# Performance work log

Hardware: AMD Instinct MI355X
Metric: run time of the kernel (lower is better)

The kernel has to match this reference:

```python
import jax, jax.numpy as jnp
import numpy as np

B, C, H, W = 8, 192, 128, 128
FILTERS = (1, 3, 3, 3, 3, 1)
BOUND = 1e-9


def setup_inputs() -> dict:
    key = jax.random.key(0)
    ks = jax.random.split(key, 16)
    d = {"x": jax.random.normal(ks[0], (B, C, H, W), jnp.float32)}
    for i in range(5):
        d[f"m{i}"] = jax.random.normal(ks[1 + i], (C, FILTERS[i + 1], FILTERS[i]), jnp.float32) * 0.5
        d[f"b{i}"] = jax.random.uniform(ks[6 + i], (C, FILTERS[i + 1], 1), jnp.float32, -0.5, 0.5)
    for i in range(4):
        d[f"f{i}"] = jax.random.normal(ks[11 + i], (C, FILTERS[i + 1], 1), jnp.float32) * 0.1
    return d


def _logits_cumulative(x, ms, bs, fs):
    # x: (C, 1, N); per-channel tiny MLP: matmul(softplus(M), x) + b, tanh gate
    logits = x
    for i in range(5):
        logits = jnp.matmul(jax.nn.softplus(ms[i]), logits) + bs[i]
        if i < 4:
            logits = logits + jnp.tanh(fs[i]) * jnp.tanh(logits)
    return logits


def reference(x, m0, m1, m2, m3, m4, b0, b1, b2, b3, b4, f0, f1, f2, f3):
    ms = (m0, m1, m2, m3, m4)
    bs = (b0, b1, b2, b3, b4)
    fs = (f0, f1, f2, f3)
    # quantize: per-sample min/max over (C,H,W), round to 16-bit grid
    x_min = jnp.min(x, axis=(1, 2, 3), keepdims=True)
    x_max = jnp.max(x, axis=(1, 2, 3), keepdims=True)
    xq = jnp.round((x - x_min) * 65535.0 / (x_max - x_min + 1e-12))
    xd = xq / 65535.0  # dequantize
    # permute (B,C,H,W)->(C,B,H,W), reshape to (C,1,N)
    xp = jnp.transpose(xd, (1, 0, 2, 3)).reshape(C, 1, -1)
    lower = _logits_cumulative(xp - 0.5, ms, bs, fs)
    upper = _logits_cumulative(xp + 0.5, ms, bs, fs)
    likelihood = jax.nn.sigmoid(upper) - jax.nn.sigmoid(lower)
    likelihood = jnp.maximum(likelihood, BOUND)  # LowerBound forward
    x_out = jnp.transpose(xp.reshape(C, B, H, W), (1, 0, 2, 3))
    likelihood = jnp.transpose(likelihood.reshape(C, B, H, W), (1, 0, 2, 3))
    return (x_out, likelihood)
```

## Files before the change

kernel.cpp:

```cpp
#include <hip/hip_runtime.h>
#include <math.h>

#define CCH 192
#define BATCH 8
#define HWSZ 16384
#define NPER (CCH * HWSZ)
#define NTOT ((size_t)BATCH * NPER)
#define INV65535 (1.0f / 65535.0f)

#define TABN    8193
#define TABSTR  8196
#define TSCALE  (8192.0f / 65535.0f)

#define WS_WTAB_OFF_FLOATS 64
#define WS_TAB_OFF_BYTES   65536
#define WS_NEEDED (WS_TAB_OFF_BYTES + (size_t)CCH * TABSTR * 4)

__device__ __forceinline__ unsigned f2u_ord(float f) {
    unsigned u = __float_as_uint(f);
    return (u & 0x80000000u) ? ~u : (u | 0x80000000u);
}
__device__ __forceinline__ float u2f_ord(unsigned u) {
    return __uint_as_float((u & 0x80000000u) ? (u ^ 0x80000000u) : ~u);
}
__device__ __forceinline__ float fexp2(float x) { return __builtin_amdgcn_exp2f(x); }
__device__ __forceinline__ float frcp(float x)  { return __builtin_amdgcn_rcpf(x); }
__device__ __forceinline__ float ftanh(float x) {
    return 1.0f - 2.0f * frcp(fexp2(2.8853900817779268f * x) + 1.0f);
}
__device__ __forceinline__ float fsig(float x) {
    return frcp(1.0f + fexp2(-1.4426950408889634f * x));
}

__global__ void setup_kernel(const float* __restrict__ m0, const float* __restrict__ b0,
                             const float* __restrict__ m1, const float* __restrict__ b1,
                             const float* __restrict__ m2, const float* __restrict__ b2,
                             const float* __restrict__ m3, const float* __restrict__ b3,
                             const float* __restrict__ m4, const float* __restrict__ b4,
                             const float* __restrict__ f0, const float* __restrict__ f1,
                             const float* __restrict__ f2, const float* __restrict__ f3,
                             unsigned* __restrict__ mm, float* __restrict__ wtab)
{
    int t = threadIdx.x;
    if (t < 8)             mm[t] = 0xFFFFFFFFu;
    if (t >= 8 && t < 16)  mm[t] = 0u;
    if (t < CCH) {
        float* w = wtab + t * 64;
        #pragma unroll
        for (int i = 0; i < 3; ++i) { float v = m0[t*3+i]; w[i]    = fmaxf(v,0.f)+log1pf(expf(-fabsf(v))); }
        #pragma unroll
        for (int i = 0; i < 9; ++i) { float v = m1[t*9+i]; w[3+i]  = fmaxf(v,0.f)+log1pf(expf(-fabsf(v))); }
        #pragma unroll
        for (int i = 0; i < 9; ++i) { float v = m2[t*9+i]; w[12+i] = fmaxf(v,0.f)+log1pf(expf(-fabsf(v))); }
        #pragma unroll
        for (int i = 0; i < 9; ++i) { float v = m3[t*9+i]; w[21+i] = fmaxf(v,0.f)+log1pf(expf(-fabsf(v))); }
        #pragma unroll
        for (int i = 0; i < 3; ++i) { float v = m4[t*3+i]; w[30+i] = fmaxf(v,0.f)+log1pf(expf(-fabsf(v))); }
        #pragma unroll
        for (int i = 0; i < 3; ++i) w[33+i] = b0[t*3+i];
        #pragma unroll
        for (int i = 0; i < 3; ++i) w[36+i] = b1[t*3+i];
        #pragma unroll
        for (int i = 0; i < 3; ++i) w[39+i] = b2[t*3+i];
        #pragma unroll
        for (int i = 0; i < 3; ++i) w[42+i] = b3[t*3+i];
        w[45] = b4[t];
        #pragma unroll
        for (int i = 0; i < 3; ++i) w[46+i] = tanhf(f0[t*3+i]);
        #pragma unroll
        for (int i = 0; i < 3; ++i) w[49+i] = tanhf(f1[t*3+i]);
        #pragma unroll
        for (int i = 0; i < 3; ++i) w[52+i] = tanhf(f2[t*3+i]);
        #pragma unroll
        for (int i = 0; i < 3; ++i) w[55+i] = tanhf(f3[t*3+i]);
    }
}

#define RED_BLOCKS_PER_SAMPLE 192
__global__ __launch_bounds__(256) void minmax_kernel(const float* __restrict__ x,
                                                     unsigned* __restrict__ mm)
{
    int b   = blockIdx.x / RED_BLOCKS_PER_SAMPLE;
    int blk = blockIdx.x % RED_BLOCKS_PER_SAMPLE;
    const float4* xs = (const float4*)(x + (size_t)b * NPER);
    int base = blk * 4096;
    float mn = INFINITY, mx = -INFINITY;
    #pragma unroll
    for (int i = 0; i < 16; ++i) {
        float4 v = xs[base + i * 256 + threadIdx.x];
        mn = fminf(mn, fminf(fminf(v.x, v.y), fminf(v.z, v.w)));
        mx = fmaxf(mx, fmaxf(fmaxf(v.x, v.y), fmaxf(v.z, v.w)));
    }
    #pragma unroll
    for (int off = 32; off > 0; off >>= 1) {
        mn = fminf(mn, __shfl_down(mn, off, 64));
        mx = fmaxf(mx, __shfl_down(mx, off, 64));
    }
    __shared__ float smn[4], smx[4];
    int wave = threadIdx.x >> 6;
    if ((threadIdx.x & 63) == 0) { smn[wave] = mn; smx[wave] = mx; }
    __syncthreads();
    if (threadIdx.x == 0) {
        #pragma unroll
        for (int i = 1; i < 4; ++i) { mn = fminf(mn, smn[i]); mx = fmaxf(mx, smx[i]); }
        atomicMin(&mm[b],     f2u_ord(mn));
        atomicMax(&mm[8 + b], f2u_ord(mx));
    }
}

__device__ __forceinline__ float eval_mlp(float x, const float* W)
{
    float a0 = fmaf(W[0], x, W[33]);
    float a1 = fmaf(W[1], x, W[34]);
    float a2 = fmaf(W[2], x, W[35]);
    a0 = fmaf(W[46], ftanh(a0), a0);
    a1 = fmaf(W[47], ftanh(a1), a1);
    a2 = fmaf(W[48], ftanh(a2), a2);

    float c0 = fmaf(W[3], a0, fmaf(W[4],  a1, fmaf(W[5],  a2, W[36])));
    float c1 = fmaf(W[6], a0, fmaf(W[7],  a1, fmaf(W[8],  a2, W[37])));
    float c2 = fmaf(W[9], a0, fmaf(W[10], a1, fmaf(W[11], a2, W[38])));
    c0 = fmaf(W[49], ftanh(c0), c0);
    c1 = fmaf(W[50], ftanh(c1), c1);
    c2 = fmaf(W[51], ftanh(c2), c2);

    float d0 = fmaf(W[12], c0, fmaf(W[13], c1, fmaf(W[14], c2, W[39])));
    float d1 = fmaf(W[15], c0, fmaf(W[16], c1, fmaf(W[17], c2, W[40])));
    float d2 = fmaf(W[18], c0, fmaf(W[19], c1, fmaf(W[20], c2, W[41])));
    d0 = fmaf(W[52], ftanh(d0), d0);
    d1 = fmaf(W[53], ftanh(d1), d1);
    d2 = fmaf(W[54], ftanh(d2), d2);

    float e0 = fmaf(W[21], d0, fmaf(W[22], d1, fmaf(W[23], d2, W[42])));
    float e1 = fmaf(W[24], d0, fmaf(W[25], d1, fmaf(W[26], d2, W[43])));
    float e2 = fmaf(W[27], d0, fmaf(W[28], d1, fmaf(W[29], d2, W[44])));
    e0 = fmaf(W[55], ftanh(e0), e0);
    e1 = fmaf(W[56], ftanh(e1), e1);
    e2 = fmaf(W[57], ftanh(e2), e2);

    return fmaf(W[30], e0, fmaf(W[31], e1, fmaf(W[32], e2, W[45])));
}

__device__ __forceinline__ float eval_lik(float d, const float* W)
{
    float lo = eval_mlp(d - 0.5f, W);
    float up = eval_mlp(d + 0.5f, W);
    return fmaxf(fsig(up) - fsig(lo), 1e-9f);
}

__global__ __launch_bounds__(256) void table_kernel(const float* __restrict__ wtab,
                                                    float* __restrict__ tab)
{
    int c = blockIdx.x / 33;
    int j = (blockIdx.x % 33) * 256 + threadIdx.x;
    if (j >= TABN) return;

    float W[58];
    const float* w = wtab + c * 64;
    #pragma unroll
    for (int i = 0; i < 58; ++i) W[i] = w[i];

    float d = (float)j * (1.0f / 8192.0f);
    tab[(size_t)c * TABSTR + j] = eval_lik(d, W);
}

__global__ __launch_bounds__(256) void gather_kernel(const float* __restrict__ x,
                                                     const unsigned* __restrict__ mm,
                                                     const float* __restrict__ tab,
                                                     float* __restrict__ out)
{
    __shared__ __align__(16) float ltab[TABN + 3];

    int c = blockIdx.x >> 3;
    int b = blockIdx.x & 7;
    int t = threadIdx.x;

    const float4* tsrc = (const float4*)(tab + (size_t)c * TABSTR);
    float4* tdst = (float4*)ltab;
    #pragma unroll
    for (int i = 0; i < 8; ++i) tdst[i * 256 + t] = tsrc[i * 256 + t];
    if (t == 0) ltab[8192] = tab[(size_t)c * TABSTR + 8192];
    __syncthreads();

    float mn = u2f_ord(mm[b]);
    float mx = u2f_ord(mm[8 + b]);
    float scale = 65535.0f / (mx - mn + 1e-12f);

    size_t base = ((size_t)b * CCH + c) * HWSZ;
    const float4* xin = (const float4*)(x + base);
    float4* o0 = (float4*)(out + base);
    float4* o1 = (float4*)(out + NTOT + base);

    auto proc = [&](float xi, float& od, float& ol) {
        float kf   = rintf((xi - mn) * scale);
        od         = kf * INV65535;
        float tpos = kf * TSCALE;
        int   j    = (int)tpos;
        j = j > 8191 ? 8191 : j;
        float frac = tpos - (float)j;
        float t0 = ltab[j];
        float t1 = ltab[j + 1];
        ol = fmaxf(fmaf(frac, t1 - t0, t0), 1e-9f);
    };

    #pragma unroll
    for (int i = 0; i < 16; ++i) {
        float4 v = xin[i * 256 + t];
        float4 xd, lk;
        proc(v.x, xd.x, lk.x);
        proc(v.y, xd.y, lk.y);
        proc(v.z, xd.z, lk.z);
        proc(v.w, xd.w, lk.w);
        o0[i * 256 + t] = xd;
        o1[i * 256 + t] = lk;
    }
}

__global__ __launch_bounds__(256) void ebott_main(const float* __restrict__ x,
                                                  const unsigned* __restrict__ mm,
                                                  const float* __restrict__ wtab,
                                                  float* __restrict__ out)
{
    int blk = blockIdx.x;
    int q   = blk & 3;
    int c   = (blk >> 2) % CCH;
    int b   = blk / (4 * CCH);

    float W[58];
    const float* w = wtab + c * 64;
    #pragma unroll
    for (int i = 0; i < 58; ++i) W[i] = w[i];

    float mn = u2f_ord(mm[b]);
    float mx = u2f_ord(mm[8 + b]);
    float scale = 65535.0f / (mx - mn + 1e-12f);

    size_t base = (size_t)(b * CCH + c) * HWSZ + q * 4096;
    const float4* xin = (const float4*)(x + base);
    float4* o0 = (float4*)(out + base);
    float4* o1 = (float4*)(out + NTOT + base);
    int t = threadIdx.x;

    auto proc = [&](float xi, float& od, float& ol) {
        float d = rintf((xi - mn) * scale) * INV65535;
        od = d;
        ol = eval_lik(d, W);
    };

    #pragma unroll
    for (int i = 0; i < 4; ++i) {
        float4 v = xin[i * 256 + t];
        float4 xd, lk;
        proc(v.x, xd.x, lk.x);
        proc(v.y, xd.y, lk.y);
        proc(v.z, xd.z, lk.z);
        proc(v.w, xd.w, lk.w);
        o0[i * 256 + t] = xd;
        o1[i * 256 + t] = lk;
    }
}

extern "C" void kernel_launch(void* const* d_in, const int* in_sizes, int n_in,
                              void* d_out, int out_size, void* d_ws, size_t ws_size,
                              hipStream_t stream)
{
    const float* x  = (const float*)d_in[0];
    const float* m0 = (const float*)d_in[1];
    const float* b0 = (const float*)d_in[2];
    const float* m1 = (const float*)d_in[3];
    const float* b1 = (const float*)d_in[4];
    const float* m2 = (const float*)d_in[5];
    const float* b2 = (const float*)d_in[6];
    const float* m3 = (const float*)d_in[7];
    const float* b3 = (const float*)d_in[8];
    const float* m4 = (const float*)d_in[9];
    const float* b4 = (const float*)d_in[10];
    const float* f0 = (const float*)d_in[11];
    const float* f1 = (const float*)d_in[12];
    const float* f2 = (const float*)d_in[13];
    const float* f3 = (const float*)d_in[14];

    unsigned* mm = (unsigned*)d_ws;
    float* wtab  = (float*)d_ws + WS_WTAB_OFF_FLOATS;
    float* tab   = (float*)((char*)d_ws + WS_TAB_OFF_BYTES);
    float* out   = (float*)d_out;

    setup_kernel<<<1, 256, 0, stream>>>(m0, b0, m1, b1, m2, b2, m3, b3, m4, b4,
                                        f0, f1, f2, f3, mm, wtab);
    minmax_kernel<<<BATCH * RED_BLOCKS_PER_SAMPLE, 256, 0, stream>>>(x, mm);

    if (ws_size >= WS_NEEDED) {
        table_kernel<<<CCH * 33, 256, 0, stream>>>(wtab, tab);
        gather_kernel<<<CCH * BATCH, 256, 0, stream>>>(x, mm, tab, out);
    } else {
        ebott_main<<<BATCH * CCH * 4, 256, 0, stream>>>(x, mm, wtab, out);
    }
}
```

Before: 358.4 us.

## Fuse setup, min/max reduction and table build into one prep kernel

Merges the single-block weight setup, the min/max reduction and the per-channel likelihood table build into one launch. Table blocks now compute their softplus/tanh weights in shared memory, while reduction blocks run alongside them. Min/max initialisation becomes a memset to 0xFF, with the max stored inverted so both reductions use atomicMin. The gather kernel switches to nontemporal loads and stores. This removes two kernel launches and their serialization, at the cost of every table block recomputing its channel weights.

```diff
diff --git a/kernel.cpp b/kernel.cpp
--- a/kernel.cpp
+++ b/kernel.cpp
@@ -16,6 +16,12 @@
 #define WS_TAB_OFF_BYTES   65536
 #define WS_NEEDED (WS_TAB_OFF_BYTES + (size_t)CCH * TABSTR * 4)
 
+#define RED_BLOCKS_PER_SAMPLE 192
+#define MINMAX_BLOCKS (BATCH * RED_BLOCKS_PER_SAMPLE)
+#define TAB_BLOCKS (CCH * 33)
+
+typedef float f4 __attribute__((ext_vector_type(4)));
+
 __device__ __forceinline__ unsigned f2u_ord(float f) {
     unsigned u = __float_as_uint(f);
     return (u & 0x80000000u) ? ~u : (u | 0x80000000u);
@@ -30,82 +36,6 @@
 }
 __device__ __forceinline__ float fsig(float x) {
     return frcp(1.0f + fexp2(-1.4426950408889634f * x));
-}
-
-__global__ void setup_kernel(const float* __restrict__ m0, const float* __restrict__ b0,
-                             const float* __restrict__ m1, const float* __restrict__ b1,
-                             const float* __restrict__ m2, const float* __restrict__ b2,
-                             const float* __restrict__ m3, const float* __restrict__ b3,
-                             const float* __restrict__ m4, const float* __restrict__ b4,
-                             const float* __restrict__ f0, const float* __restrict__ f1,
-                             const float* __restrict__ f2, const float* __restrict__ f3,
-                             unsigned* __restrict__ mm, float* __restrict__ wtab)
-{
-    int t = threadIdx.x;
-    if (t < 8)             mm[t] = 0xFFFFFFFFu;
-    if (t >= 8 && t < 16)  mm[t] = 0u;
-    if (t < CCH) {
-        float* w = wtab + t * 64;
-        #pragma unroll
-        for (int i = 0; i < 3; ++i) { float v = m0[t*3+i]; w[i]    = fmaxf(v,0.f)+log1pf(expf(-fabsf(v))); }
-        #pragma unroll
-        for (int i = 0; i < 9; ++i) { float v = m1[t*9+i]; w[3+i]  = fmaxf(v,0.f)+log1pf(expf(-fabsf(v))); }
-        #pragma unroll
-        for (int i = 0; i < 9; ++i) { float v = m2[t*9+i]; w[12+i] = fmaxf(v,0.f)+log1pf(expf(-fabsf(v))); }
-        #pragma unroll
-        for (int i = 0; i < 9; ++i) { float v = m3[t*9+i]; w[21+i] = fmaxf(v,0.f)+log1pf(expf(-fabsf(v))); }
-        #pragma unroll
-        for (int i = 0; i < 3; ++i) { float v = m4[t*3+i]; w[30+i] = fmaxf(v,0.f)+log1pf(expf(-fabsf(v))); }
-        #pragma unroll
-        for (int i = 0; i < 3; ++i) w[33+i] = b0[t*3+i];
-        #pragma unroll
-        for (int i = 0; i < 3; ++i) w[36+i] = b1[t*3+i];
-        #pragma unroll
-        for (int i = 0; i < 3; ++i) w[39+i] = b2[t*3+i];
-        #pragma unroll
-        for (int i = 0; i < 3; ++i) w[42+i] = b3[t*3+i];
-        w[45] = b4[t];
-        #pragma unroll
-        for (int i = 0; i < 3; ++i) w[46+i] = tanhf(f0[t*3+i]);
-        #pragma unroll
-        for (int i = 0; i < 3; ++i) w[49+i] = tanhf(f1[t*3+i]);
-        #pragma unroll
-        for (int i = 0; i < 3; ++i) w[52+i] = tanhf(f2[t*3+i]);
-        #pragma unroll
-        for (int i = 0; i < 3; ++i) w[55+i] = tanhf(f3[t*3+i]);
-    }
-}
-
-#define RED_BLOCKS_PER_SAMPLE 192
-__global__ __launch_bounds__(256) void minmax_kernel(const float* __restrict__ x,
-                                                     unsigned* __restrict__ mm)
-{
-    int b   = blockIdx.x / RED_BLOCKS_PER_SAMPLE;
-    int blk = blockIdx.x % RED_BLOCKS_PER_SAMPLE;
-    const float4* xs = (const float4*)(x + (size_t)b * NPER);
-    int base = blk * 4096;
-    float mn = INFINITY, mx = -INFINITY;
-    #pragma unroll
-    for (int i = 0; i < 16; ++i) {
-        float4 v = xs[base + i * 256 + threadIdx.x];
-        mn = fminf(mn, fminf(fminf(v.x, v.y), fminf(v.z, v.w)));
-        mx = fmaxf(mx, fmaxf(fmaxf(v.x, v.y), fmaxf(v.z, v.w)));
-    }
-    #pragma unroll
-    for (int off = 32; off > 0; off >>= 1) {
-        mn = fminf(mn, __shfl_down(mn, off, 64));
-        mx = fmaxf(mx, __shfl_down(mx, off, 64));
-    }
-    __shared__ float smn[4], smx[4];
-    int wave = threadIdx.x >> 6;
-    if ((threadIdx.x & 63) == 0) { smn[wave] = mn; smx[wave] = mx; }
-    __syncthreads();
-    if (threadIdx.x == 0) {
-        #pragma unroll
-        for (int i = 1; i < 4; ++i) { mn = fminf(mn, smn[i]); mx = fmaxf(mx, smx[i]); }
-        atomicMin(&mm[b],     f2u_ord(mn));
-        atomicMax(&mm[8 + b], f2u_ord(mx));
-    }
 }
 
 __device__ __forceinline__ float eval_mlp(float x, const float* W)
@@ -148,20 +78,96 @@
     return fmaxf(fsig(up) - fsig(lo), 1e-9f);
 }
 
-__global__ __launch_bounds__(256) void table_kernel(const float* __restrict__ wtab,
-                                                    float* __restrict__ tab)
-{
-    int c = blockIdx.x / 33;
-    int j = (blockIdx.x % 33) * 256 + threadIdx.x;
-    if (j >= TABN) return;
+__device__ __forceinline__ void minmax_block(const float* __restrict__ x,
+                                             unsigned* __restrict__ mm,
+                                             int bid)
+{
+    int b   = bid / RED_BLOCKS_PER_SAMPLE;
+    int blk = bid % RED_BLOCKS_PER_SAMPLE;
+    const f4* xs = (const f4*)(x + (size_t)b * NPER);
+    int base = blk * 4096;
+    float mn = INFINITY, mx = -INFINITY;
+    #pragma unroll
+    for (int i = 0; i < 16; ++i) {
+        f4 v = xs[base + i * 256 + threadIdx.x];
+        mn = fminf(mn, fminf(fminf(v.x, v.y), fminf(v.z, v.w)));
+        mx = fmaxf(mx, fmaxf(fmaxf(v.x, v.y), fmaxf(v.z, v.w)));
+    }
+    #pragma unroll
+    for (int off = 32; off > 0; off >>= 1) {
+        mn = fminf(mn, __shfl_down(mn, off, 64));
+        mx = fmaxf(mx, __shfl_down(mx, off, 64));
+    }
+    __shared__ float smn[4], smx[4];
+    int wave = threadIdx.x >> 6;
+    if ((threadIdx.x & 63) == 0) { smn[wave] = mn; smx[wave] = mx; }
+    __syncthreads();
+    if (threadIdx.x == 0) {
+        #pragma unroll
+        for (int i = 1; i < 4; ++i) { mn = fminf(mn, smn[i]); mx = fmaxf(mx, smx[i]); }
+        atomicMin(&mm[b],     f2u_ord(mn));
+        atomicMin(&mm[8 + b], ~f2u_ord(mx));
+    }
+}
+
+__global__ __launch_bounds__(256) void prep_kernel(
+    const float* __restrict__ x, unsigned* __restrict__ mm,
+    const float* __restrict__ m0, const float* __restrict__ b0,
+    const float* __restrict__ m1, const float* __restrict__ b1,
+    const float* __restrict__ m2, const float* __restrict__ b2,
+    const float* __restrict__ m3, const float* __restrict__ b3,
+    const float* __restrict__ m4, const float* __restrict__ b4,
+    const float* __restrict__ f0, const float* __restrict__ f1,
+    const float* __restrict__ f2, const float* __restrict__ f3,
+    float* __restrict__ tab)
+{
+    if (blockIdx.x < MINMAX_BLOCKS) {
+        minmax_block(x, mm, blockIdx.x);
+        return;
+    }
+    int tb = blockIdx.x - MINMAX_BLOCKS;
+    int c  = tb / 33;
+    int jc = tb % 33;
+    int t  = threadIdx.x;
+
+    __shared__ float sW[58];
+    if (t < 58) {
+        float v;
+        if (t < 33) {
+            if      (t < 3)  v = m0[c * 3 + t];
+            else if (t < 12) v = m1[c * 9 + t - 3];
+            else if (t < 21) v = m2[c * 9 + t - 12];
+            else if (t < 30) v = m3[c * 9 + t - 21];
+            else             v = m4[c * 3 + t - 30];
+            v = fmaxf(v, 0.f) + log1pf(expf(-fabsf(v)));
+        } else if (t < 46) {
+            int i = t - 33;
+            if      (i < 3)  v = b0[c * 3 + i];
+            else if (i < 6)  v = b1[c * 3 + i - 3];
+            else if (i < 9)  v = b2[c * 3 + i - 6];
+            else if (i < 12) v = b3[c * 3 + i - 9];
+            else             v = b4[c];
+        } else {
+            int i = t - 46;
+            if      (i < 3)  v = f0[c * 3 + i];
+            else if (i < 6)  v = f1[c * 3 + i - 3];
+            else if (i < 9)  v = f2[c * 3 + i - 6];
+            else             v = f3[c * 3 + i - 9];
+            v = tanhf(v);
+        }
+        sW[t] = v;
+    }
+    __syncthreads();
 
     float W[58];
-    const float* w = wtab + c * 64;
-    #pragma unroll
-    for (int i = 0; i < 58; ++i) W[i] = w[i];
-
-    float d = (float)j * (1.0f / 8192.0f);
-    tab[(size_t)c * TABSTR + j] = eval_lik(d, W);
+    #pragma unroll
+    for (int i = 0; i < 58; ++i) W[i] = sW[i];
+
+    int j = jc * 256 + t;
+    if (j < TABN) {
+        float d = (float)j * (1.0f / 8192.0f);
+        tab[(size_t)c * TABSTR + j] = eval_lik(d, W);
+    }
 }
 
 __global__ __launch_bounds__(256) void gather_kernel(const float* __restrict__ x,
@@ -175,21 +181,21 @@
     int b = blockIdx.x & 7;
     int t = threadIdx.x;
 
-    const float4* tsrc = (const float4*)(tab + (size_t)c * TABSTR);
-    float4* tdst = (float4*)ltab;
+    const f4* tsrc = (const f4*)(tab + (size_t)c * TABSTR);
+    f4* tdst = (f4*)ltab;
     #pragma unroll
     for (int i = 0; i < 8; ++i) tdst[i * 256 + t] = tsrc[i * 256 + t];
     if (t == 0) ltab[8192] = tab[(size_t)c * TABSTR + 8192];
     __syncthreads();
 
     float mn = u2f_ord(mm[b]);
-    float mx = u2f_ord(mm[8 + b]);
+    float mx = u2f_ord(~mm[8 + b]);
     float scale = 65535.0f / (mx - mn + 1e-12f);
 
     size_t base = ((size_t)b * CCH + c) * HWSZ;
-    const float4* xin = (const float4*)(x + base);
-    float4* o0 = (float4*)(out + base);
-    float4* o1 = (float4*)(out + NTOT + base);
+    const f4* xin = (const f4*)(x + base);
+    f4* o0 = (f4*)(out + base);
+    f4* o1 = (f4*)(out + NTOT + base);
 
     auto proc = [&](float xi, float& od, float& ol) {
         float kf   = rintf((xi - mn) * scale);
@@ -205,14 +211,57 @@
 
     #pragma unroll
     for (int i = 0; i < 16; ++i) {
-        float4 v = xin[i * 256 + t];
-        float4 xd, lk;
-        proc(v.x, xd.x, lk.x);
-        proc(v.y, xd.y, lk.y);
-        proc(v.z, xd.z, lk.z);
-        proc(v.w, xd.w, lk.w);
-        o0[i * 256 + t] = xd;
-        o1[i * 256 + t] = lk;
+        f4 v = __builtin_nontemporal_load(&xin[i * 256 + t]);
+        float in[4] = {v.x, v.y, v.z, v.w};
+        float xd[4], lk[4];
+        #pragma unroll
+        for (int k = 0; k < 4; ++k) proc(in[k], xd[k], lk[k]);
+        f4 vxd = {xd[0], xd[1], xd[2], xd[3]};
+        f4 vlk = {lk[0], lk[1], lk[2], lk[3]};
+        __builtin_nontemporal_store(vxd, &o0[i * 256 + t]);
+        __builtin_nontemporal_store(vlk, &o1[i * 256 + t]);
+    }
+}
+
+__global__ void setup_kernel(const float* __restrict__ m0, const float* __restrict__ b0,
+                             const float* __restrict__ m1, const float* __restrict__ b1,
+                             const float* __restrict__ m2, const float* __restrict__ b2,
+                             const float* __restrict__ m3, const float* __restrict__ b3,
+                             const float* __restrict__ m4, const float* __restrict__ b4,
+                             const float* __restrict__ f0, const float* __restrict__ f1,
+                             const float* __restrict__ f2, const float* __restrict__ f3,
+                             float* __restrict__ wtab)
+{
+    int t = threadIdx.x;
+    if (t < CCH) {
+        float* w = wtab + t * 64;
+        #pragma unroll
+        for (int i = 0; i < 3; ++i) { float v = m0[t*3+i]; w[i]    = fmaxf(v,0.f)+log1pf(expf(-fabsf(v))); }
+        #pragma unroll
+        for (int i = 0; i < 9; ++i) { float v = m1[t*9+i]; w[3+i]  = fmaxf(v,0.f)+log1pf(expf(-fabsf(v))); }
+        #pragma unroll
+        for (int i = 0; i < 9; ++i) { float v = m2[t*9+i]; w[12+i] = fmaxf(v,0.f)+log1pf(expf(-fabsf(v))); }
+        #pragma unroll
+        for (int i = 0; i < 9; ++i) { float v = m3[t*9+i]; w[21+i] = fmaxf(v,0.f)+log1pf(expf(-fabsf(v))); }
+        #pragma unroll
+        for (int i = 0; i < 3; ++i) { float v = m4[t*3+i]; w[30+i] = fmaxf(v,0.f)+log1pf(expf(-fabsf(v))); }
+        #pragma unroll
+        for (int i = 0; i < 3; ++i) w[33+i] = b0[t*3+i];
+        #pragma unroll
+        for (int i = 0; i < 3; ++i) w[36+i] = b1[t*3+i];
+        #pragma unroll
+        for (int i = 0; i < 3; ++i) w[39+i] = b2[t*3+i];
+        #pragma unroll
+        for (int i = 0; i < 3; ++i) w[42+i] = b3[t*3+i];
+        w[45] = b4[t];
+        #pragma unroll
+        for (int i = 0; i < 3; ++i) w[46+i] = tanhf(f0[t*3+i]);
+        #pragma unroll
+        for (int i = 0; i < 3; ++i) w[49+i] = tanhf(f1[t*3+i]);
+        #pragma unroll
+        for (int i = 0; i < 3; ++i) w[52+i] = tanhf(f2[t*3+i]);
+        #pragma unroll
+        for (int i = 0; i < 3; ++i) w[55+i] = tanhf(f3[t*3+i]);
     }
 }
 
@@ -232,31 +281,30 @@
     for (int i = 0; i < 58; ++i) W[i] = w[i];
 
     float mn = u2f_ord(mm[b]);
-    float mx = u2f_ord(mm[8 + b]);
+    float mx = u2f_ord(~mm[8 + b]);
     float scale = 65535.0f / (mx - mn + 1e-12f);
 
     size_t base = (size_t)(b * CCH + c) * HWSZ + q * 4096;
-    const float4* xin = (const float4*)(x + base);
-    float4* o0 = (float4*)(out + base);
-    float4* o1 = (float4*)(out + NTOT + base);
+    const f4* xin = (const f4*)(x + base);
+    f4* o0 = (f4*)(out + base);
+    f4* o1 = (f4*)(out + NTOT + base);
     int t = threadIdx.x;
 
-    auto proc = [&](float xi, float& od, float& ol) {
-        float d = rintf((xi - mn) * scale) * INV65535;
-        od = d;
-        ol = eval_lik(d, W);
-    };
-
     #pragma unroll
     for (int i = 0; i < 4; ++i) {
-        float4 v = xin[i * 256 + t];
-        float4 xd, lk;
-        proc(v.x, xd.x, lk.x);
-        proc(v.y, xd.y, lk.y);
-        proc(v.z, xd.z, lk.z);
-        proc(v.w, xd.w, lk.w);
-        o0[i * 256 + t] = xd;
-        o1[i * 256 + t] = lk;
+        f4 v = xin[i * 256 + t];
+        float in[4] = {v.x, v.y, v.z, v.w};
+        float xd[4], lk[4];
+        #pragma unroll
+        for (int k = 0; k < 4; ++k) {
+            float d = rintf((in[k] - mn) * scale) * INV65535;
+            xd[k] = d;
+            lk[k] = eval_lik(d, W);
+        }
+        f4 vxd = {xd[0], xd[1], xd[2], xd[3]};
+        f4 vlk = {lk[0], lk[1], lk[2], lk[3]};
+        o0[i * 256 + t] = vxd;
+        o1[i * 256 + t] = vlk;
     }
 }
 
@@ -285,14 +333,17 @@
     float* tab   = (float*)((char*)d_ws + WS_TAB_OFF_BYTES);
     float* out   = (float*)d_out;
 
-    setup_kernel<<<1, 256, 0, stream>>>(m0, b0, m1, b1, m2, b2, m3, b3, m4, b4,
-                                        f0, f1, f2, f3, mm, wtab);
-    minmax_kernel<<<BATCH * RED_BLOCKS_PER_SAMPLE, 256, 0, stream>>>(x, mm);
+    hipMemsetAsync(d_ws, 0xFF, 64, stream);
 
     if (ws_size >= WS_NEEDED) {
-        table_kernel<<<CCH * 33, 256, 0, stream>>>(wtab, tab);
+        prep_kernel<<<MINMAX_BLOCKS + TAB_BLOCKS, 256, 0, stream>>>(
+            x, mm, m0, b0, m1, b1, m2, b2, m3, b3, m4, b4, f0, f1, f2, f3, tab);
         gather_kernel<<<CCH * BATCH, 256, 0, stream>>>(x, mm, tab, out);
     } else {
+        setup_kernel<<<1, 256, 0, stream>>>(m0, b0, m1, b1, m2, b2, m3, b3, m4, b4,
+                                            f0, f1, f2, f3, wtab);
+        prep_kernel<<<MINMAX_BLOCKS, 256, 0, stream>>>(
+            x, mm, m0, b0, m1, b1, m2, b2, m3, b3, m4, b4, f0, f1, f2, f3, tab);
         ebott_main<<<BATCH * CCH * 4, 256, 0, stream>>>(x, mm, wtab, out);
     }
 }
```

Measured after the change: 337.4 us. -5.9%, faster.
